# Optimization experiments

Measured on AMD Instinct MI355X. Metric: run time of the kernel, lower is better.

## Reference

```python
import jax, jax.numpy as jnp
import numpy as np
from jax import lax

B, L, D = 8, 2048, 512


def _mlp(x, w1, w2):
    # MemoryMLP: x + gelu(x @ w1) @ w2  (exact gelu, matching F.gelu default)
    return x + jax.nn.gelu(x @ w1, approximate=False) @ w2


def _l2norm(t):
    # F.normalize(p=2, dim=-1, eps=1e-12)
    n = jnp.linalg.norm(t, axis=-1, keepdims=True)
    return t / jnp.maximum(n, 1e-12)


def setup_inputs() -> dict:
    key = jax.random.key(0)
    ks = jax.random.split(key, 12)
    s = 0.02
    return {
        "x": jax.random.normal(ks[0], (B, L, D), jnp.float32),
        "conv_w": jax.random.normal(ks[1], (D, 1, 4), jnp.float32) * s,  # depthwise, (out, in/groups, k)
        "conv_b": jax.random.normal(ks[2], (D,), jnp.float32) * s,
        "q_w": jax.random.normal(ks[3], (D, D), jnp.float32) * s,  # Linear weight (out, in)
        "mem_w1": jax.random.normal(ks[4], (D, D), jnp.float32) * s,
        "mem_w2": jax.random.normal(ks[5], (D, D), jnp.float32) * s,
        "eta_w1": jax.random.normal(ks[6], (D, D), jnp.float32) * s,
        "eta_w2": jax.random.normal(ks[7], (D, D), jnp.float32) * s,
        "alpha_w1": jax.random.normal(ks[8], (D, D), jnp.float32) * s,
        "alpha_w2": jax.random.normal(ks[9], (D, D), jnp.float32) * s,
    }


def _forward(x, conv_w, conv_b, q_w, mem_w1, mem_w2, eta_w1, eta_w2, alpha_w1, alpha_w2):
    # causal depthwise conv: Conv1d(k=4, padding=3, groups=D) then slice [:L] == left-pad 3
    xc = lax.conv_general_dilated(
        jnp.transpose(x, (0, 2, 1)),  # (B, D, L)
        conv_w,                        # (D, 1, 4)
        window_strides=(1,),
        padding=[(3, 0)],
        feature_group_count=D,
        dimension_numbers=("NCH", "OIH", "NCH"),
    ) + conv_b[None, :, None]
    xc = jnp.transpose(xc, (0, 2, 1))  # (B, L, D)

    # time-invariant branches (m_k/m_v weights are never updated; kt/vt/hat_v do not
    # affect the output, so they are elided). q, eta, alpha use fixed weights -> vectorize.
    q = _l2norm(xc @ q_w.T)                                   # (B, L, D)
    eta_mean = jax.nn.sigmoid(_mlp(xc, eta_w1, eta_w2)).mean(axis=(0, 2))      # (L,)
    alpha_mean = jax.nn.sigmoid(_mlp(xc, alpha_w1, alpha_w2)).mean(axis=(0, 2))  # (L,)

    def step(carry, inp):
        w1, w2 = carry
        q_t, a_t, e_t = inp  # (B, D), (), ()
        o_t = _mlp(q_t, w1, w2)  # output uses pre-update memory
        new_w1 = w1 * a_t - e_t * 0.01
        new_w2 = w2 * a_t - e_t * 0.01
        return (new_w1, new_w2), o_t

    qs = jnp.transpose(q, (1, 0, 2))  # (L, B, D)
    (_, _), outs = lax.scan(step, (mem_w1, mem_w2), (qs, alpha_mean, eta_mean))
    return jnp.transpose(outs, (1, 0, 2))  # (B, L, D)


def reference(x, conv_w, conv_b, q_w, mem_w1, mem_w2, eta_w1, eta_w2, alpha_w1, alpha_w2):
    return _forward(x, conv_w, conv_b, q_w, mem_w1, mem_w2, eta_w1, eta_w2, alpha_w1, alpha_w2)
```

## Files before the change

kernel.cpp:

```cpp
#include <hip/hip_runtime.h>
#include <math.h>

constexpr int Bn = 8, Ln = 2048, Dn = 512;
constexpr int Mn = Bn * Ln;

typedef __bf16 bf16x8 __attribute__((ext_vector_type(8)));
typedef __bf16 bf16x4v __attribute__((ext_vector_type(4)));
typedef __bf16 bf16x2v __attribute__((ext_vector_type(2)));
typedef float f32x4 __attribute__((ext_vector_type(4)));

__device__ __forceinline__ float gelu_exact(float x) {
    return 0.5f * x * (1.0f + erff(x * 0.7071067811865475f));
}
__device__ __forceinline__ float sigmoid_f(float x) {
    return 1.0f / (1.0f + expf(-x));
}

__global__ __launch_bounds__(256) void conv_kernel(
    const float* __restrict__ x, const float* __restrict__ w,
    const float* __restrict__ bias, __bf16* __restrict__ xcb) {
    int idx = blockIdx.x * 256 + threadIdx.x;
    int g = idx & 127;
    int bl = idx >> 7;
    int l = bl & (Ln - 1);
    int d = g * 4;
    float a[4];
    float4 b4 = *(const float4*)&bias[d];
    a[0] = b4.x; a[1] = b4.y; a[2] = b4.z; a[3] = b4.w;
    float wv[16];
    *(float4*)&wv[0]  = *(const float4*)&w[d * 4];
    *(float4*)&wv[4]  = *(const float4*)&w[d * 4 + 4];
    *(float4*)&wv[8]  = *(const float4*)&w[d * 4 + 8];
    *(float4*)&wv[12] = *(const float4*)&w[d * 4 + 12];
#pragma unroll
    for (int k = 0; k < 4; ++k) {
        int ll = l - 3 + k;
        if (ll >= 0) {
            float4 xv = *(const float4*)&x[(size_t)(bl - 3 + k) * Dn + d];
            a[0] += xv.x * wv[0 * 4 + k];
            a[1] += xv.y * wv[1 * 4 + k];
            a[2] += xv.z * wv[2 * 4 + k];
            a[3] += xv.w * wv[3 * 4 + k];
        }
    }
    bf16x4v o = { (__bf16)a[0], (__bf16)a[1], (__bf16)a[2], (__bf16)a[3] };
    *(bf16x4v*)&xcb[(size_t)bl * Dn + d] = o;
}

__global__ __launch_bounds__(256) void wconv_kernel(
    const float* __restrict__ ew1, const float* __restrict__ aw1,
    const float* __restrict__ ew2, const float* __restrict__ aw2,
    const float* __restrict__ mw1, const float* __restrict__ mw2,
    const float* __restrict__ qw,
    __bf16* __restrict__ Wht, __bf16* __restrict__ W2t,
    __bf16* __restrict__ m1t, __bf16* __restrict__ m2t,
    __bf16* __restrict__ qwt) {
    __shared__ float tile[64][65];
    int z = blockIdx.z;
    const float* src;
    __bf16* dst;
    int trans = 1;
    switch (z) {
        case 0: src = ew1; dst = Wht; break;
        case 1: src = aw1; dst = Wht + 512 * 512; break;
        case 2: src = ew2; dst = W2t; break;
        case 3: src = aw2; dst = W2t + 512 * 512; break;
        case 4: src = mw1; dst = m1t; break;
        case 5: src = mw2; dst = m2t; break;
        default: src = qw; dst = qwt; trans = 0; break;
    }
    int r0 = blockIdx.y * 64, c0 = blockIdx.x * 64;
    if (!trans) {
        for (int i = threadIdx.x; i < 4096; i += 256) {
            int r = i >> 6, c = i & 63;
            dst[(size_t)(r0 + r) * 512 + c0 + c] = (__bf16)src[(size_t)(r0 + r) * 512 + c0 + c];
        }
        return;
    }
    for (int i = threadIdx.x; i < 4096; i += 256) {
        int r = i >> 6, c = i & 63;
        tile[r][c] = src[(size_t)(r0 + r) * 512 + c0 + c];
    }
    __syncthreads();
    for (int i = threadIdx.x; i < 4096; i += 256) {
        int r = i >> 6, c = i & 63;
        dst[(size_t)(c0 + r) * 512 + r0 + c] = (__bf16)tile[c][r];
    }
}

template <int OP>
__global__ __launch_bounds__(256, 2) void gemm_mfma(
    const __bf16* __restrict__ A, int lda, int Az,
    const __bf16* __restrict__ Bt, int Bz,
    void* __restrict__ Cptr, int ldc,
    const __bf16* __restrict__ auxb,
    const float* __restrict__ Pv, const float* __restrict__ Qv,
    const float* __restrict__ Rv,
    float* __restrict__ red) {
    __shared__ __align__(16) __bf16 Asl[128 * 32];
    __shared__ __align__(16) __bf16 Bsl[128 * 32];
    const int tid = threadIdx.x;
    const int lane = tid & 63, wv = tid >> 6;
    const int wm = wv & 1, wn = wv >> 1;
    const int fr = lane & 15, fq = lane >> 4;
    const int z = blockIdx.z;
    A += (size_t)z * Az;
    Bt += (size_t)z * Bz;
    const __bf16* Ab = A + (size_t)blockIdx.y * 128 * lda;
    const __bf16* Bb = Bt + (size_t)blockIdx.x * 128 * 512;
    float* redp = (OP == 1) ? red + (size_t)z * Ln : red;

    f32x4 acc[4][4] = {};

    for (int k0 = 0; k0 < 512; k0 += 32) {
#pragma unroll
        for (int i = 0; i < 2; ++i) {
            int c = tid + i * 256;
            int r = c >> 2, co = (c & 3) * 8;
            __builtin_amdgcn_global_load_lds(
                (const __attribute__((address_space(1))) void*)(Ab + (size_t)r * lda + k0 + co),
                (__attribute__((address_space(3))) void*)(Asl + c * 8), 16, 0, 0);
            __builtin_amdgcn_global_load_lds(
                (const __attribute__((address_space(1))) void*)(Bb + (size_t)r * 512 + k0 + co),
                (__attribute__((address_space(3))) void*)(Bsl + c * 8), 16, 0, 0);
        }
        __syncthreads();
        bf16x8 af[4], bfr[4];
#pragma unroll
        for (int mi = 0; mi < 4; ++mi)
            af[mi] = *(const bf16x8*)&Asl[(wm * 64 + mi * 16 + fr) * 32 + fq * 8];
#pragma unroll
        for (int ni = 0; ni < 4; ++ni)
            bfr[ni] = *(const bf16x8*)&Bsl[(wn * 64 + ni * 16 + fr) * 32 + fq * 8];
#pragma unroll
        for (int mi = 0; mi < 4; ++mi)
#pragma unroll
            for (int ni = 0; ni < 4; ++ni)
                acc[mi][ni] = __builtin_amdgcn_mfma_f32_16x16x32_bf16(af[mi], bfr[ni], acc[mi][ni], 0, 0, 0);
        __syncthreads();
    }

    const int row_base = blockIdx.y * 128 + wm * 64;
    const int col_base = blockIdx.x * 128 + wn * 64;
#pragma unroll
    for (int mi = 0; mi < 4; ++mi) {
#pragma unroll
        for (int r = 0; r < 4; ++r) {
            int row = row_base + mi * 16 + fq * 4 + r;
            float p = 0.f, qs = 0.f, rs = 0.f;
            if (OP >= 3) { int t = row & (Ln - 1); p = Pv[t]; qs = Qv[t]; rs = Rv[row]; }
            float s = 0.f;
#pragma unroll
            for (int ni = 0; ni < 4; ++ni) {
                int col = col_base + ni * 16 + fr;
                float v = acc[mi][ni][r];
                if (OP == 0) v = gelu_exact(v);
                else if (OP == 1) v = sigmoid_f((float)auxb[(size_t)row * 512 + col] + v);
                else if (OP == 3) v = gelu_exact(p * v + qs * rs);
                else if (OP == 4) v = (float)auxb[(size_t)row * 512 + col] + p * v + qs * rs;
                if (OP == 0 || OP == 2 || OP == 3)
                    ((__bf16*)Cptr)[(size_t)row * ldc + col] = (__bf16)v;
                else if (OP == 4)
                    ((float*)Cptr)[(size_t)row * ldc + col] = v;
                s += v;
            }
            if (OP == 1 || OP == 3) {
                s += __shfl_xor(s, 1, 64);
                s += __shfl_xor(s, 2, 64);
                s += __shfl_xor(s, 4, 64);
                s += __shfl_xor(s, 8, 64);
                if (fr == 0) {
                    if (OP == 1) atomicAdd(&redp[row & (Ln - 1)], s * (1.0f / 4096.0f));
                    else atomicAdd(&redp[row], s);
                }
            }
        }
    }
}

__device__ __forceinline__ float block_reduce_sum256(float v, float* sred) {
#pragma unroll
    for (int o = 32; o > 0; o >>= 1) v += __shfl_xor(v, o, 64);
    int lane = threadIdx.x & 63, w = threadIdx.x >> 6;
    if (lane == 0) sred[w] = v;
    __syncthreads();
    float r = sred[0] + sred[1] + sred[2] + sred[3];
    __syncthreads();
    return r;
}

__global__ __launch_bounds__(256) void scan_kernel(const float* __restrict__ a,
                                                   const float* __restrict__ e,
                                                   float* __restrict__ P,
                                                   float* __restrict__ Q) {
    int tid = threadIdx.x;
    int base = tid * 8;
    float la[8], le[8], Aloc[8], Bloc[8];
#pragma unroll
    for (int j = 0; j < 8; ++j) { la[j] = a[base + j]; le[j] = e[base + j]; }
    float Ac = 1.f, Bc = 0.f;
#pragma unroll
    for (int j = 0; j < 8; ++j) {
        Aloc[j] = Ac; Bloc[j] = Bc;
        Bc = Bc * la[j] - 0.01f * le[j];
        Ac *= la[j];
    }
    float Aw = Ac, Bw = Bc;
#pragma unroll
    for (int off = 1; off < 64; off <<= 1) {
        float Ap = __shfl_up(Aw, off, 64);
        float Bp = __shfl_up(Bw, off, 64);
        if ((tid & 63) >= off) { Bw = Aw * Bp + Bw; Aw = Aw * Ap; }
    }
    __shared__ float wA[4], wB[4];
    if ((tid & 63) == 63) { wA[tid >> 6] = Aw; wB[tid >> 6] = Bw; }
    __syncthreads();
    float Apre = 1.f, Bpre = 0.f;
    for (int w = 0; w < (tid >> 6); ++w) { Bpre = wA[w] * Bpre + wB[w]; Apre = wA[w] * Apre; }
    float Ax = __shfl_up(Aw, 1, 64), Bx = __shfl_up(Bw, 1, 64);
    if ((tid & 63) == 0) { Ax = 1.f; Bx = 0.f; }
    float At = Ax * Apre, Bt2 = Ax * Bpre + Bx;
#pragma unroll
    for (int j = 0; j < 8; ++j) {
        P[base + j] = Aloc[j] * At;
        Q[base + j] = Aloc[j] * Bt2 + Bloc[j];
    }
}

__global__ __launch_bounds__(256) void l2norm_kernel(__bf16* __restrict__ q,
                                                     float* __restrict__ S) {
    __shared__ float sred[4];
    int n = blockIdx.x, tid = threadIdx.x;
    __bf16* row = q + (size_t)n * Dn;
    bf16x2v v = ((bf16x2v*)row)[tid];
    float f0 = (float)v.x, f1 = (float)v.y;
    float ss = block_reduce_sum256(f0 * f0 + f1 * f1, sred);
    float sc = 1.f / fmaxf(sqrtf(ss), 1e-12f);
    f0 *= sc; f1 *= sc;
    float rs = block_reduce_sum256(f0 + f1, sred);
    bf16x2v o = { (__bf16)f0, (__bf16)f1 };
    ((bf16x2v*)row)[tid] = o;
    if (!tid) S[n] = rs;
}

extern "C" void kernel_launch(void* const* d_in, const int* in_sizes, int n_in,
                              void* d_out, int out_size, void* d_ws, size_t ws_size,
                              hipStream_t stream) {
    const float* x        = (const float*)d_in[0];
    const float* conv_w   = (const float*)d_in[1];
    const float* conv_b   = (const float*)d_in[2];
    const float* q_w      = (const float*)d_in[3];
    const float* mem_w1   = (const float*)d_in[4];
    const float* mem_w2   = (const float*)d_in[5];
    const float* eta_w1   = (const float*)d_in[6];
    const float* eta_w2   = (const float*)d_in[7];
    const float* alpha_w1 = (const float*)d_in[8];
    const float* alpha_w2 = (const float*)d_in[9];
    float* out = (float*)d_out;

    char* w = (char*)d_ws;
    __bf16* xcb = (__bf16*)w;     w += (size_t)Mn * Dn * 2;
    __bf16* H   = (__bf16*)w;     w += (size_t)Mn * 1024 * 2;
    __bf16* qb  = (__bf16*)w;     w += (size_t)Mn * Dn * 2;
    __bf16* G   = (__bf16*)w;     w += (size_t)Mn * Dn * 2;
    __bf16* Wht = (__bf16*)w;     w += (size_t)1024 * 512 * 2;
    __bf16* W2t = (__bf16*)w;     w += (size_t)2 * 512 * 512 * 2;
    __bf16* qwt = (__bf16*)w;     w += (size_t)512 * 512 * 2;
    __bf16* m1t = (__bf16*)w;     w += (size_t)512 * 512 * 2;
    __bf16* m2t = (__bf16*)w;     w += (size_t)512 * 512 * 2;
    float* Rv      = (float*)w;   w += (size_t)Mn * 4;
    float* MeanAcc = (float*)w;   w += (size_t)2 * Ln * 4;
    float* Pv = (float*)w;        w += Ln * 4;
    float* Qv = (float*)w;        w += Ln * 4;
    float* Sv = (float*)w;        w += (size_t)Mn * 4;

    hipMemsetAsync(Rv, 0, (size_t)(Mn + 2 * Ln) * 4, stream);

    conv_kernel<<<Mn * Dn / 4 / 256, 256, 0, stream>>>(x, conv_w, conv_b, xcb);
    wconv_kernel<<<dim3(8, 8, 7), 256, 0, stream>>>(eta_w1, alpha_w1, eta_w2, alpha_w2,
                                                    mem_w1, mem_w2, q_w,
                                                    Wht, W2t, m1t, m2t, qwt);
    gemm_mfma<0><<<dim3(8, 128, 1), 256, 0, stream>>>(xcb, 512, 0, Wht, 0,
                                                      H, 1024, nullptr, nullptr, nullptr, nullptr, nullptr);
    gemm_mfma<1><<<dim3(4, 128, 2), 256, 0, stream>>>(H, 1024, 512, W2t, 512 * 512,
                                                      nullptr, 0, xcb, nullptr, nullptr, nullptr, MeanAcc);
    scan_kernel<<<1, 256, 0, stream>>>(MeanAcc + Ln, MeanAcc, Pv, Qv);
    gemm_mfma<2><<<dim3(4, 128, 1), 256, 0, stream>>>(xcb, 512, 0, qwt, 0,
                                                      qb, 512, nullptr, nullptr, nullptr, nullptr, nullptr);
    l2norm_kernel<<<Mn, 256, 0, stream>>>(qb, Sv);
    gemm_mfma<3><<<dim3(4, 128, 1), 256, 0, stream>>>(qb, 512, 0, m1t, 0,
                                                      G, 512, nullptr, Pv, Qv, Sv, Rv);
    gemm_mfma<4><<<dim3(4, 128, 1), 256, 0, stream>>>(G, 512, 0, m2t, 0,
                                                      out, 512, qb, Pv, Qv, Rv, nullptr);
}
```

Baseline: 283.2 us.

## Fuse q projection into first GEMM and fold l2norm into downstream epilogues

```diff
diff --git a/kernel.cpp b/kernel.cpp
--- a/kernel.cpp
+++ b/kernel.cpp
@@ -3,73 +3,74 @@
 
 constexpr int Bn = 8, Ln = 2048, Dn = 512;
 constexpr int Mn = Bn * Ln;
+constexpr int CONV_BLOCKS = Mn * Dn / 4 / 256;
 
 typedef __bf16 bf16x8 __attribute__((ext_vector_type(8)));
 typedef __bf16 bf16x4v __attribute__((ext_vector_type(4)));
-typedef __bf16 bf16x2v __attribute__((ext_vector_type(2)));
 typedef float f32x4 __attribute__((ext_vector_type(4)));
 
 __device__ __forceinline__ float gelu_exact(float x) {
     return 0.5f * x * (1.0f + erff(x * 0.7071067811865475f));
 }
-__device__ __forceinline__ float sigmoid_f(float x) {
-    return 1.0f / (1.0f + expf(-x));
-}
-
-__global__ __launch_bounds__(256) void conv_kernel(
+__device__ __forceinline__ float sigmoid_fast(float x) {
+    return __builtin_amdgcn_rcpf(1.0f + __expf(-x));
+}
+
+__global__ __launch_bounds__(256) void prep_kernel(
     const float* __restrict__ x, const float* __restrict__ w,
-    const float* __restrict__ bias, __bf16* __restrict__ xcb) {
-    int idx = blockIdx.x * 256 + threadIdx.x;
-    int g = idx & 127;
-    int bl = idx >> 7;
-    int l = bl & (Ln - 1);
-    int d = g * 4;
-    float a[4];
-    float4 b4 = *(const float4*)&bias[d];
-    a[0] = b4.x; a[1] = b4.y; a[2] = b4.z; a[3] = b4.w;
-    float wv[16];
-    *(float4*)&wv[0]  = *(const float4*)&w[d * 4];
-    *(float4*)&wv[4]  = *(const float4*)&w[d * 4 + 4];
-    *(float4*)&wv[8]  = *(const float4*)&w[d * 4 + 8];
-    *(float4*)&wv[12] = *(const float4*)&w[d * 4 + 12];
-#pragma unroll
-    for (int k = 0; k < 4; ++k) {
-        int ll = l - 3 + k;
-        if (ll >= 0) {
-            float4 xv = *(const float4*)&x[(size_t)(bl - 3 + k) * Dn + d];
-            a[0] += xv.x * wv[0 * 4 + k];
-            a[1] += xv.y * wv[1 * 4 + k];
-            a[2] += xv.z * wv[2 * 4 + k];
-            a[3] += xv.w * wv[3 * 4 + k];
-        }
-    }
-    bf16x4v o = { (__bf16)a[0], (__bf16)a[1], (__bf16)a[2], (__bf16)a[3] };
-    *(bf16x4v*)&xcb[(size_t)bl * Dn + d] = o;
-}
-
-__global__ __launch_bounds__(256) void wconv_kernel(
+    const float* __restrict__ bias, __bf16* __restrict__ xcb,
     const float* __restrict__ ew1, const float* __restrict__ aw1,
     const float* __restrict__ ew2, const float* __restrict__ aw2,
     const float* __restrict__ mw1, const float* __restrict__ mw2,
     const float* __restrict__ qw,
-    __bf16* __restrict__ Wht, __bf16* __restrict__ W2t,
-    __bf16* __restrict__ m1t, __bf16* __restrict__ m2t,
-    __bf16* __restrict__ qwt) {
+    __bf16* __restrict__ Wall, __bf16* __restrict__ W2t,
+    __bf16* __restrict__ m1t, __bf16* __restrict__ m2t) {
     __shared__ float tile[64][65];
-    int z = blockIdx.z;
+    if (blockIdx.x < CONV_BLOCKS) {
+        int idx = blockIdx.x * 256 + threadIdx.x;
+        int g = idx & 127;
+        int bl = idx >> 7;
+        int l = bl & (Ln - 1);
+        int d = g * 4;
+        float a[4];
+        float4 b4 = *(const float4*)&bias[d];
+        a[0] = b4.x; a[1] = b4.y; a[2] = b4.z; a[3] = b4.w;
+        float wv[16];
+        *(float4*)&wv[0]  = *(const float4*)&w[d * 4];
+        *(float4*)&wv[4]  = *(const float4*)&w[d * 4 + 4];
+        *(float4*)&wv[8]  = *(const float4*)&w[d * 4 + 8];
+        *(float4*)&wv[12] = *(const float4*)&w[d * 4 + 12];
+#pragma unroll
+        for (int k = 0; k < 4; ++k) {
+            int ll = l - 3 + k;
+            if (ll >= 0) {
+                float4 xv = *(const float4*)&x[(size_t)(bl - 3 + k) * Dn + d];
+                a[0] += xv.x * wv[0 * 4 + k];
+                a[1] += xv.y * wv[1 * 4 + k];
+                a[2] += xv.z * wv[2 * 4 + k];
+                a[3] += xv.w * wv[3 * 4 + k];
+            }
+        }
+        bf16x4v o = { (__bf16)a[0], (__bf16)a[1], (__bf16)a[2], (__bf16)a[3] };
+        *(bf16x4v*)&xcb[(size_t)bl * Dn + d] = o;
+        return;
+    }
+    int bid = blockIdx.x - CONV_BLOCKS;
+    int z = bid >> 6;
+    int t = bid & 63;
+    int r0 = (t >> 3) * 64, c0 = (t & 7) * 64;
     const float* src;
     __bf16* dst;
     int trans = 1;
     switch (z) {
-        case 0: src = ew1; dst = Wht; break;
-        case 1: src = aw1; dst = Wht + 512 * 512; break;
+        case 0: src = ew1; dst = Wall; break;
+        case 1: src = aw1; dst = Wall + 512 * 512; break;
         case 2: src = ew2; dst = W2t; break;
         case 3: src = aw2; dst = W2t + 512 * 512; break;
         case 4: src = mw1; dst = m1t; break;
         case 5: src = mw2; dst = m2t; break;
-        default: src = qw; dst = qwt; trans = 0; break;
-    }
-    int r0 = blockIdx.y * 64, c0 = blockIdx.x * 64;
+        default: src = qw; dst = Wall + 1024 * 512; trans = 0; break;
+    }
     if (!trans) {
         for (int i = threadIdx.x; i < 4096; i += 256) {
             int r = i >> 6, c = i & 63;
@@ -88,16 +89,18 @@
     }
 }
 
-template <int OP>
+template <int OP, int BM>
 __global__ __launch_bounds__(256, 2) void gemm_mfma(
     const __bf16* __restrict__ A, int lda, int Az,
     const __bf16* __restrict__ Bt, int Bz,
-    void* __restrict__ Cptr, int ldc,
+    void* __restrict__ C0, void* __restrict__ C1,
     const __bf16* __restrict__ auxb,
     const float* __restrict__ Pv, const float* __restrict__ Qv,
-    const float* __restrict__ Rv,
-    float* __restrict__ red) {
-    __shared__ __align__(16) __bf16 Asl[128 * 32];
+    const float* __restrict__ SSv, const float* __restrict__ RSv,
+    float* __restrict__ red0, float* __restrict__ red1, float* __restrict__ red2) {
+    constexpr int MI = BM / 32;
+    constexpr int AISS = BM / 64;
+    __shared__ __align__(16) __bf16 Asl[BM * 32];
     __shared__ __align__(16) __bf16 Bsl[128 * 32];
     const int tid = threadIdx.x;
     const int lane = tid & 63, wv = tid >> 6;
@@ -106,87 +109,104 @@
     const int z = blockIdx.z;
     A += (size_t)z * Az;
     Bt += (size_t)z * Bz;
-    const __bf16* Ab = A + (size_t)blockIdx.y * 128 * lda;
+    const __bf16* Ab = A + (size_t)blockIdx.y * BM * lda;
     const __bf16* Bb = Bt + (size_t)blockIdx.x * 128 * 512;
-    float* redp = (OP == 1) ? red + (size_t)z * Ln : red;
-
-    f32x4 acc[4][4] = {};
+    float* redp = (OP == 1) ? red0 + (size_t)z * Ln : red0;
+
+    f32x4 acc[MI][4] = {};
 
     for (int k0 = 0; k0 < 512; k0 += 32) {
 #pragma unroll
-        for (int i = 0; i < 2; ++i) {
+        for (int i = 0; i < AISS; ++i) {
             int c = tid + i * 256;
             int r = c >> 2, co = (c & 3) * 8;
             __builtin_amdgcn_global_load_lds(
                 (const __attribute__((address_space(1))) void*)(Ab + (size_t)r * lda + k0 + co),
                 (__attribute__((address_space(3))) void*)(Asl + c * 8), 16, 0, 0);
+        }
+#pragma unroll
+        for (int i = 0; i < 2; ++i) {
+            int c = tid + i * 256;
+            int r = c >> 2, co = (c & 3) * 8;
             __builtin_amdgcn_global_load_lds(
                 (const __attribute__((address_space(1))) void*)(Bb + (size_t)r * 512 + k0 + co),
                 (__attribute__((address_space(3))) void*)(Bsl + c * 8), 16, 0, 0);
         }
         __syncthreads();
-        bf16x8 af[4], bfr[4];
-#pragma unroll
-        for (int mi = 0; mi < 4; ++mi)
-            af[mi] = *(const bf16x8*)&Asl[(wm * 64 + mi * 16 + fr) * 32 + fq * 8];
+        bf16x8 af[MI], bfr[4];
+#pragma unroll
+        for (int mi = 0; mi < MI; ++mi)
+            af[mi] = *(const bf16x8*)&Asl[(wm * (BM / 2) + mi * 16 + fr) * 32 + fq * 8];
 #pragma unroll
         for (int ni = 0; ni < 4; ++ni)
             bfr[ni] = *(const bf16x8*)&Bsl[(wn * 64 + ni * 16 + fr) * 32 + fq * 8];
 #pragma unroll
-        for (int mi = 0; mi < 4; ++mi)
+        for (int mi = 0; mi < MI; ++mi)
 #pragma unroll
             for (int ni = 0; ni < 4; ++ni)
                 acc[mi][ni] = __builtin_amdgcn_mfma_f32_16x16x32_bf16(af[mi], bfr[ni], acc[mi][ni], 0, 0, 0);
         __syncthreads();
     }
 
-    const int row_base = blockIdx.y * 128 + wm * 64;
+    const int row_base = blockIdx.y * BM + wm * (BM / 2);
     const int col_base = blockIdx.x * 128 + wn * 64;
-#pragma unroll
-    for (int mi = 0; mi < 4; ++mi) {
+    const bool qpath = (OP == 0) && (blockIdx.x >= 8);
+#pragma unroll
+    for (int mi = 0; mi < MI; ++mi) {
 #pragma unroll
         for (int r = 0; r < 4; ++r) {
             int row = row_base + mi * 16 + fq * 4 + r;
-            float p = 0.f, qs = 0.f, rs = 0.f;
-            if (OP >= 3) { int t = row & (Ln - 1); p = Pv[t]; qs = Qv[t]; rs = Rv[row]; }
-            float s = 0.f;
+            float p = 0.f, qs = 0.f, rs = 0.f, inv = 1.f;
+            if (OP >= 3) {
+                int t = row & (Ln - 1);
+                p = Pv[t]; qs = Qv[t];
+                rs = RSv[row];
+                inv = 1.0f / fmaxf(sqrtf(SSv[row]), 1e-12f);
+            }
+            float s1 = 0.f, s2 = 0.f;
 #pragma unroll
             for (int ni = 0; ni < 4; ++ni) {
                 int col = col_base + ni * 16 + fr;
                 float v = acc[mi][ni][r];
-                if (OP == 0) v = gelu_exact(v);
-                else if (OP == 1) v = sigmoid_f((float)auxb[(size_t)row * 512 + col] + v);
-                else if (OP == 3) v = gelu_exact(p * v + qs * rs);
-                else if (OP == 4) v = (float)auxb[(size_t)row * 512 + col] + p * v + qs * rs;
-                if (OP == 0 || OP == 2 || OP == 3)
-                    ((__bf16*)Cptr)[(size_t)row * ldc + col] = (__bf16)v;
-                else if (OP == 4)
-                    ((float*)Cptr)[(size_t)row * ldc + col] = v;
-                s += v;
-            }
-            if (OP == 1 || OP == 3) {
-                s += __shfl_xor(s, 1, 64);
-                s += __shfl_xor(s, 2, 64);
-                s += __shfl_xor(s, 4, 64);
-                s += __shfl_xor(s, 8, 64);
+                if (OP == 0) {
+                    if (!qpath) {
+                        v = gelu_exact(v);
+                        ((__bf16*)C0)[(size_t)row * 1024 + col] = (__bf16)v;
+                    } else {
+                        ((__bf16*)C1)[(size_t)row * 512 + col - 1024] = (__bf16)v;
+                        s1 += v; s2 += v * v;
+                    }
+                } else if (OP == 1) {
+                    v = sigmoid_fast((float)auxb[(size_t)row * 512 + col] + v);
+                    s1 += v;
+                } else if (OP == 3) {
+                    v = gelu_exact(inv * (p * v + qs * rs));
+                    ((__bf16*)C0)[(size_t)row * 512 + col] = (__bf16)v;
+                    s1 += v;
+                } else if (OP == 4) {
+                    float qn = (float)auxb[(size_t)row * 512 + col] * inv;
+                    ((float*)C0)[(size_t)row * 512 + col] = qn + p * v + qs * rs;
+                }
+            }
+            if (OP == 1 || OP == 3 || (OP == 0 && qpath)) {
+                s1 += __shfl_xor(s1, 1, 64);
+                s1 += __shfl_xor(s1, 2, 64);
+                s1 += __shfl_xor(s1, 4, 64);
+                s1 += __shfl_xor(s1, 8, 64);
+                if (OP == 0) {
+                    s2 += __shfl_xor(s2, 1, 64);
+                    s2 += __shfl_xor(s2, 2, 64);
+                    s2 += __shfl_xor(s2, 4, 64);
+                    s2 += __shfl_xor(s2, 8, 64);
+                }
                 if (fr == 0) {
-                    if (OP == 1) atomicAdd(&redp[row & (Ln - 1)], s * (1.0f / 4096.0f));
-                    else atomicAdd(&redp[row], s);
+                    if (OP == 1) atomicAdd(&redp[row & (Ln - 1)], s1 * (1.0f / 4096.0f));
+                    else if (OP == 3) atomicAdd(&red0[row], s1);
+                    else { atomicAdd(&red1[row], s2); atomicAdd(&red2[row], s1); }
                 }
             }
         }
     }
-}
-
-__device__ __forceinline__ float block_reduce_sum256(float v, float* sred) {
-#pragma unroll
-    for (int o = 32; o > 0; o >>= 1) v += __shfl_xor(v, o, 64);
-    int lane = threadIdx.x & 63, w = threadIdx.x >> 6;
-    if (lane == 0) sred[w] = v;
-    __syncthreads();
-    float r = sred[0] + sred[1] + sred[2] + sred[3];
-    __syncthreads();
-    return r;
 }
 
 __global__ __launch_bounds__(256) void scan_kernel(const float* __restrict__ a,
@@ -225,22 +245,6 @@
         P[base + j] = Aloc[j] * At;
         Q[base + j] = Aloc[j] * Bt2 + Bloc[j];
     }
-}
-
-__global__ __launch_bounds__(256) void l2norm_kernel(__bf16* __restrict__ q,
-                                                     float* __restrict__ S) {
-    __shared__ float sred[4];
-    int n = blockIdx.x, tid = threadIdx.x;
-    __bf16* row = q + (size_t)n * Dn;
-    bf16x2v v = ((bf16x2v*)row)[tid];
-    float f0 = (float)v.x, f1 = (float)v.y;
-    float ss = block_reduce_sum256(f0 * f0 + f1 * f1, sred);
-    float sc = 1.f / fmaxf(sqrtf(ss), 1e-12f);
-    f0 *= sc; f1 *= sc;
-    float rs = block_reduce_sum256(f0 + f1, sred);
-    bf16x2v o = { (__bf16)f0, (__bf16)f1 };
-    ((bf16x2v*)row)[tid] = o;
-    if (!tid) S[n] = rs;
 }
 
 extern "C" void kernel_launch(void* const* d_in, const int* in_sizes, int n_in,
@@ -259,37 +263,37 @@
     float* out = (float*)d_out;
 
     char* w = (char*)d_ws;
-    __bf16* xcb = (__bf16*)w;     w += (size_t)Mn * Dn * 2;
-    __bf16* H   = (__bf16*)w;     w += (size_t)Mn * 1024 * 2;
-    __bf16* qb  = (__bf16*)w;     w += (size_t)Mn * Dn * 2;
-    __bf16* G   = (__bf16*)w;     w += (size_t)Mn * Dn * 2;
-    __bf16* Wht = (__bf16*)w;     w += (size_t)1024 * 512 * 2;
-    __bf16* W2t = (__bf16*)w;     w += (size_t)2 * 512 * 512 * 2;
-    __bf16* qwt = (__bf16*)w;     w += (size_t)512 * 512 * 2;
-    __bf16* m1t = (__bf16*)w;     w += (size_t)512 * 512 * 2;
-    __bf16* m2t = (__bf16*)w;     w += (size_t)512 * 512 * 2;
+    __bf16* xcb  = (__bf16*)w;    w += (size_t)Mn * Dn * 2;
+    __bf16* H    = (__bf16*)w;    w += (size_t)Mn * 1024 * 2;
+    __bf16* qb   = (__bf16*)w;    w += (size_t)Mn * Dn * 2;
+    __bf16* G    = (__bf16*)w;    w += (size_t)Mn * Dn * 2;
+    __bf16* Wall = (__bf16*)w;    w += (size_t)1536 * 512 * 2;
+    __bf16* W2t  = (__bf16*)w;    w += (size_t)2 * 512 * 512 * 2;
+    __bf16* m1t  = (__bf16*)w;    w += (size_t)512 * 512 * 2;
+    __bf16* m2t  = (__bf16*)w;    w += (size_t)512 * 512 * 2;
     float* Rv      = (float*)w;   w += (size_t)Mn * 4;
     float* MeanAcc = (float*)w;   w += (size_t)2 * Ln * 4;
+    float* SS      = (float*)w;   w += (size_t)Mn * 4;
+    float* RS      = (float*)w;   w += (size_t)Mn * 4;
     float* Pv = (float*)w;        w += Ln * 4;
     float* Qv = (float*)w;        w += Ln * 4;
-    float* Sv = (float*)w;        w += (size_t)Mn * 4;
-
-    hipMemsetAsync(Rv, 0, (size_t)(Mn + 2 * Ln) * 4, stream);
-
-    conv_kernel<<<Mn * Dn / 4 / 256, 256, 0, stream>>>(x, conv_w, conv_b, xcb);
-    wconv_kernel<<<dim3(8, 8, 7), 256, 0, stream>>>(eta_w1, alpha_w1, eta_w2, alpha_w2,
-                                                    mem_w1, mem_w2, q_w,
-                                                    Wht, W2t, m1t, m2t, qwt);
-    gemm_mfma<0><<<dim3(8, 128, 1), 256, 0, stream>>>(xcb, 512, 0, Wht, 0,
-                                                      H, 1024, nullptr, nullptr, nullptr, nullptr, nullptr);
-    gemm_mfma<1><<<dim3(4, 128, 2), 256, 0, stream>>>(H, 1024, 512, W2t, 512 * 512,
-                                                      nullptr, 0, xcb, nullptr, nullptr, nullptr, MeanAcc);
+
+    hipMemsetAsync(Rv, 0, (size_t)(Mn + 2 * Ln + Mn + Mn) * 4, stream);
+
+    prep_kernel<<<CONV_BLOCKS + 448, 256, 0, stream>>>(
+        x, conv_w, conv_b, xcb, eta_w1, alpha_w1, eta_w2, alpha_w2,
+        mem_w1, mem_w2, q_w, Wall, W2t, m1t, m2t);
+    gemm_mfma<0, 128><<<dim3(12, 128), 256, 0, stream>>>(
+        xcb, 512, 0, Wall, 0, H, qb, nullptr,
+        nullptr, nullptr, nullptr, nullptr, nullptr, SS, RS);
+    gemm_mfma<1, 128><<<dim3(4, 128, 2), 256, 0, stream>>>(
+        H, 1024, 512, W2t, 512 * 512, nullptr, nullptr, xcb,
+        nullptr, nullptr, nullptr, nullptr, MeanAcc, nullptr, nullptr);
     scan_kernel<<<1, 256, 0, stream>>>(MeanAcc + Ln, MeanAcc, Pv, Qv);
-    gemm_mfma<2><<<dim3(4, 128, 1), 256, 0, stream>>>(xcb, 512, 0, qwt, 0,
-                                                      qb, 512, nullptr, nullptr, nullptr, nullptr, nullptr);
-    l2norm_kernel<<<Mn, 256, 0, stream>>>(qb, Sv);
-    gemm_mfma<3><<<dim3(4, 128, 1), 256, 0, stream>>>(qb, 512, 0, m1t, 0,
-                                                      G, 512, nullptr, Pv, Qv, Sv, Rv);
-    gemm_mfma<4><<<dim3(4, 128, 1), 256, 0, stream>>>(G, 512, 0, m2t, 0,
-                                                      out, 512, qb, Pv, Qv, Rv, nullptr);
-}
+    gemm_mfma<3, 64><<<dim3(4, 256), 256, 0, stream>>>(
+        qb, 512, 0, m1t, 0, G, nullptr, nullptr,
+        Pv, Qv, SS, RS, Rv, nullptr, nullptr);
+    gemm_mfma<4, 64><<<dim3(4, 256), 256, 0, stream>>>(
+        G, 512, 0, m2t, 0, out, nullptr, qb,
+        Pv, Qv, SS, Rv, nullptr, nullptr, nullptr);
+}
```

New measurement: 263.0 us. -7.1%, faster.
